# Kernel optimization log

Measured on AMD Instinct MI355X. Metric: run time of the kernel, lower is better.

The kernel has to match this reference:

```python
import jax, jax.numpy as jnp
import numpy as np

B, S = 256, 2048
VOCAB, E, H, OUT = 10, 32, 64, 10


def setup_inputs() -> dict:
    key = jax.random.key(0)
    ks = jax.random.split(key, 8)
    num1 = jax.random.randint(ks[0], (B, S), 0, VOCAB, dtype=jnp.int32)
    num2 = jax.random.randint(ks[1], (B, S), 0, VOCAB, dtype=jnp.int32)
    embed = jax.random.normal(ks[2], (VOCAB, E), dtype=jnp.float32) * 0.05
    Wx = jax.random.normal(ks[3], (2 * E, H), dtype=jnp.float32) * (1.0 / np.sqrt(2 * E))
    Wh = jax.random.normal(ks[4], (H, H), dtype=jnp.float32) * (1.0 / np.sqrt(H))
    b = jnp.zeros((H,), dtype=jnp.float32)
    Wd = jax.random.normal(ks[5], (H, OUT), dtype=jnp.float32) * (1.0 / np.sqrt(H))
    bd = jnp.zeros((OUT,), dtype=jnp.float32)
    return {"num1": num1, "num2": num2, "embed": embed, "Wx": Wx,
            "Wh": Wh, "b": b, "Wd": Wd, "bd": bd}


def reference(num1, num2, embed, Wx, Wh, b, Wd, bd):
    # embedding lookup + concat -> [B, S, 2E]
    x = jnp.concatenate([embed[num1], embed[num2]], axis=2)
    # precompute input projection once (big GEMM), scan only the recurrence
    xw = jnp.einsum('bse,eh->bsh', x, Wx) + b  # [B, S, H]

    def step(h, xw_t):
        h = jnp.tanh(xw_t + h @ Wh)  # SimpleRNNCell: tanh(x W + h U + b)
        return h, h

    h0 = jnp.zeros((x.shape[0], Wh.shape[0]), dtype=x.dtype)
    _, hs = jax.lax.scan(step, h0, jnp.swapaxes(xw, 0, 1))  # hs: [S, B, H]
    hs = jnp.swapaxes(hs, 0, 1)  # [B, S, H]
    logits = jnp.einsum('bsh,ho->bso', hs, Wd) + bd  # [B, S, 10]
    return logits
```

## Files before the change

### kernel.cpp

```cpp
#include <hip/hip_runtime.h>

namespace {
typedef float v2f __attribute__((ext_vector_type(2)));
typedef unsigned u32x2 __attribute__((ext_vector_type(2)));
constexpr int kB = 256;
constexpr int kS = 2048;
constexpr int kV = 10;
constexpr int kE = 32;
constexpr int kH = 64;
constexpr int kO = 10;
constexpr int kT = 16;
constexpr int kPad = 68;
constexpr int kTiles = kS / kT;
constexpr float kC = 2.885390081777927f;

__device__ __forceinline__ float step_tanh(float s) {
    s = __builtin_amdgcn_fmed3f(s, -26.f, 26.f);
    float e = __builtin_amdgcn_exp2f(s);
    float r = __builtin_amdgcn_rcpf(e + 1.f);
    return fmaf(-2.f, r, 1.f);
}

__device__ __forceinline__ float swap32(float p) {
    u32x2 r = __builtin_amdgcn_permlane32_swap(__float_as_uint(p),
                                               __float_as_uint(p),
                                               false, false);
    return (__uint_as_float(r.x) + __uint_as_float(r.y)) - p;
}

__device__ __forceinline__ void do_logits(const float* __restrict__ hb,
                                          const float (* __restrict__ WdT)[kPad],
                                          const float* __restrict__ bdL,
                                          float* __restrict__ out, int obase, int l)
{
    #pragma unroll
    for (int r = 0; r < 3; ++r) {
        int f = r * 64 + l;
        if (f < kT * kO) {
            int tl = f / kO;
            int o  = f - tl * kO;
            const float4* hb4 = reinterpret_cast<const float4*>(hb + tl * kPad);
            const float4* wd4 = reinterpret_cast<const float4*>(&WdT[o][0]);
            float a0 = bdL[o], a1 = 0.f, a2 = 0.f, a3 = 0.f;
            #pragma unroll
            for (int c = 0; c < kH / 4; ++c) {
                float4 h4 = hb4[c];
                float4 w4 = wd4[c];
                a0 = fmaf(h4.x, w4.x, a0);
                a1 = fmaf(h4.y, w4.y, a1);
                a2 = fmaf(h4.z, w4.z, a2);
                a3 = fmaf(h4.w, w4.w, a3);
            }
            out[obase + f] = (a0 + a1) + (a2 + a3);
        }
    }
}

__global__ __launch_bounds__(128, 1)
void rnn_fused(const int* __restrict__ num1, const int* __restrict__ num2,
               const float* __restrict__ embed, const float* __restrict__ Wx,
               const float* __restrict__ Wh, const float* __restrict__ bias,
               const float* __restrict__ Wd, const float* __restrict__ bd,
               float* __restrict__ out)
{
    const int row = blockIdx.x;
    const int tid = threadIdx.x;
    const int w   = tid >> 6;
    const int l   = tid & 63;
    const int lx  = l ^ 32;
    const int kbase = (l >> 5) * 32;

    __shared__ __align__(16) float TT[kV * kV][kH];
    __shared__ __align__(16) float hbuf[2][kT][kPad];
    __shared__ __align__(16) float WdT[kO][kPad];
    __shared__ float bdL[kO];

    v2f whcA2[kH / 4], whcB2[kH / 4];
    int idx_next = 0;
    const int lane16 = l & 15;
    const int nb = row * kS;
    const int orow = row * (kS * kO);

    if (w == 0) {
        float wxc[2 * kE];
        #pragma unroll
        for (int k = 0; k < 2 * kE; ++k) wxc[k] = Wx[k * kH + l];
        float bj = bias[l];
        float t1[kV], t2[kV];
        #pragma unroll
        for (int v = 0; v < kV; ++v) {
            float a0 = 0.f, a1 = 0.f;
            #pragma unroll
            for (int k = 0; k < kE; ++k) {
                float e = embed[v * kE + k];
                a0 = fmaf(e, wxc[k], a0);
                a1 = fmaf(e, wxc[kE + k], a1);
            }
            t1[v] = a0; t2[v] = a1;
        }
        #pragma unroll
        for (int v1 = 0; v1 < kV; ++v1)
            #pragma unroll
            for (int v2 = 0; v2 < kV; ++v2)
                TT[v1 * kV + v2][l] = kC * (t1[v1] + t2[v2] + bj);
        #pragma unroll
        for (int i = 0; i < kH / 4; ++i) {
            v2f ta, tb;
            ta.x = kC * Wh[(kbase + 2 * i)     * kH + l];
            ta.y = kC * Wh[(kbase + 2 * i + 1) * kH + l];
            tb.x = kC * Wh[(kbase + 2 * i)     * kH + lx];
            tb.y = kC * Wh[(kbase + 2 * i + 1) * kH + lx];
            whcA2[i] = ta; whcB2[i] = tb;
        }
        hbuf[1][kT - 1][l] = 0.f;
        idx_next = num1[nb + lane16] * kV + num2[nb + lane16];
        __builtin_amdgcn_s_setprio(1);
    } else {
        #pragma unroll
        for (int o = 0; o < kO; ++o) WdT[o][l] = Wd[l * kO + o];
        if (l < kO) bdL[l] = bd[l];
    }
    __syncthreads();

    const float* prevRow = &hbuf[1][kT - 1][0];

    for (int ti = 0; ti < kTiles; ++ti) {
        if (w == 0) {
            const int idxv = idx_next;
            if (ti + 1 < kTiles) {
                int tt = nb + (ti + 1) * kT + lane16;
                idx_next = num1[tt] * kV + num2[tt];
            }
            float* curBase = &hbuf[ti & 1][0][0];
            #pragma unroll 1
            for (int tl = 0; tl < kT; ++tl) {
                const int sidx = __builtin_amdgcn_readlane(idxv, tl);
                const float xwv = TT[sidx][l];
                const float4* hq = reinterpret_cast<const float4*>(prevRow + kbase);
                float4 q[8];
                #pragma unroll
                for (int c = 0; c < 8; ++c) q[c] = hq[c];
                __builtin_amdgcn_sched_barrier(0);
                v2f o0; o0.x = xwv; o0.y = 0.f;
                v2f o1 = {0.f, 0.f}, r0 = {0.f, 0.f}, r1 = {0.f, 0.f};
                #pragma unroll
                for (int c = 0; c < 8; ++c) {
                    v2f lo; lo.x = q[c].x; lo.y = q[c].y;
                    v2f hi; hi.x = q[c].z; hi.y = q[c].w;
                    o0 = lo * whcA2[2 * c]     + o0;
                    o1 = hi * whcA2[2 * c + 1] + o1;
                    r0 = lo * whcB2[2 * c]     + r0;
                    r1 = hi * whcB2[2 * c + 1] + r1;
                }
                v2f rv = r0 + r1;  float pPar = rv.x + rv.y;
                float oth = swap32(pPar);
                v2f ov = o0 + o1;  float pOwn = ov.x + ov.y;
                float hcur = step_tanh(pOwn + oth);
                float* wr = curBase + tl * kPad;
                wr[l] = hcur;
                prevRow = wr;
            }
        } else if (ti > 0) {
            do_logits(&hbuf[(ti - 1) & 1][0][0], WdT, bdL, out,
                      orow + (ti - 1) * kT * kO, l);
        }
        __syncthreads();
    }
    if (w == 1)
        do_logits(&hbuf[(kTiles - 1) & 1][0][0], WdT, bdL, out,
                  orow + (kS - kT) * kO, l);
}
}

extern "C" void kernel_launch(void* const* d_in, const int* in_sizes, int n_in,
                              void* d_out, int out_size, void* d_ws, size_t ws_size,
                              hipStream_t stream) {
    (void)in_sizes; (void)n_in; (void)d_ws; (void)ws_size; (void)out_size;
    rnn_fused<<<dim3(kB), dim3(128), 0, stream>>>(
        (const int*)d_in[0], (const int*)d_in[1],
        (const float*)d_in[2], (const float*)d_in[3],
        (const float*)d_in[4], (const float*)d_in[5],
        (const float*)d_in[6], (const float*)d_in[7],
        (float*)d_out);
}
```

Baseline: 456.2 us.

## Keep RNN hidden state in registers and exchange via DPP row rotations

Replaces the per-step write and re-read of the hidden state through shared memory with cross-lane exchanges. Each step rotates h within 16-lane rows using DPP row_ror. Partial sums are then combined with permlane16/permlane32 swaps. Wh is loaded into registers in a rotated layout to match the DPP pattern. The goal is to take LDS store-to-load latency off the serial recurrence critical path, at the cost of more cross-lane ops, more FMAs and select logic per step.

After: 509.7 us. 11.7% more time.

```diff
diff --git a/kernel.cpp b/kernel.cpp
--- a/kernel.cpp
+++ b/kernel.cpp
@@ -27,6 +27,21 @@
                                                false, false);
     return (__uint_as_float(r.x) + __uint_as_float(r.y)) - p;
 }
+
+#if __has_builtin(__builtin_amdgcn_permlane16_swap)
+__device__ __forceinline__ float sum16(float p) {
+    u32x2 r = __builtin_amdgcn_permlane16_swap(__float_as_uint(p),
+                                               __float_as_uint(p),
+                                               false, false);
+    return __uint_as_float(r.x) + __uint_as_float(r.y);
+}
+#else
+__device__ __forceinline__ float sum16(float p) {
+    float o = __int_as_float(
+        __builtin_amdgcn_ds_swizzle(__float_as_int(p), 0x401F));
+    return p + o;
+}
+#endif
 
 __device__ __forceinline__ void do_logits(const float* __restrict__ hb,
                                           const float (* __restrict__ WdT)[kPad],
@@ -67,17 +82,19 @@
     const int tid = threadIdx.x;
     const int w   = tid >> 6;
     const int l   = tid & 63;
-    const int lx  = l ^ 32;
-    const int kbase = (l >> 5) * 32;
+    const int b   = l & 15;
+    const int q   = l >> 4;
 
     __shared__ __align__(16) float TT[kV * kV][kH];
     __shared__ __align__(16) float hbuf[2][kT][kPad];
     __shared__ __align__(16) float WdT[kO][kPad];
     __shared__ float bdL[kO];
 
-    v2f whcA2[kH / 4], whcB2[kH / 4];
+    v2f wA[16], wB[16];
+    float h = 0.f;
     int idx_next = 0;
-    const int lane16 = l & 15;
+    bool qb0 = false, qb1 = false;
+    const int lane16 = b;
     const int nb = row * kS;
     const int orow = row * (kS * kO);
 
@@ -103,16 +120,22 @@
             #pragma unroll
             for (int v2 = 0; v2 < kV; ++v2)
                 TT[v1 * kV + v2][l] = kC * (t1[v1] + t2[v2] + bj);
-        #pragma unroll
-        for (int i = 0; i < kH / 4; ++i) {
-            v2f ta, tb;
-            ta.x = kC * Wh[(kbase + 2 * i)     * kH + l];
-            ta.y = kC * Wh[(kbase + 2 * i + 1) * kH + l];
-            tb.x = kC * Wh[(kbase + 2 * i)     * kH + lx];
-            tb.y = kC * Wh[(kbase + 2 * i + 1) * kH + lx];
-            whcA2[i] = ta; whcB2[i] = tb;
-        }
-        hbuf[1][kT - 1][l] = 0.f;
+
+        #define SETW(i, SRC)                                                \
+            do { int s_ = (SRC);                                            \
+                 const float* p_ = Wh + s_ * kH + b;                        \
+                 wA[i].x = kC * p_[0];  wA[i].y = kC * p_[16];              \
+                 wB[i].x = kC * p_[32]; wB[i].y = kC * p_[48]; } while (0)
+        SETW(0, l);
+        #define SETR(i) SETW(i, __builtin_amdgcn_mov_dpp(l, 0x120 + i, 0xf, 0xf, false))
+        SETR(1);  SETR(2);  SETR(3);  SETR(4);  SETR(5);
+        SETR(6);  SETR(7);  SETR(8);  SETR(9);  SETR(10);
+        SETR(11); SETR(12); SETR(13); SETR(14); SETR(15);
+        #undef SETR
+        #undef SETW
+
+        qb0 = (q & 1) != 0;
+        qb1 = (q & 2) != 0;
         idx_next = num1[nb + lane16] * kV + num2[nb + lane16];
         __builtin_amdgcn_s_setprio(1);
     } else {
@@ -121,8 +144,6 @@
         if (l < kO) bdL[l] = bd[l];
     }
     __syncthreads();
-
-    const float* prevRow = &hbuf[1][kT - 1][0];
 
     for (int ti = 0; ti < kTiles; ++ti) {
         if (w == 0) {
@@ -136,29 +157,35 @@
             for (int tl = 0; tl < kT; ++tl) {
                 const int sidx = __builtin_amdgcn_readlane(idxv, tl);
                 const float xwv = TT[sidx][l];
-                const float4* hq = reinterpret_cast<const float4*>(prevRow + kbase);
-                float4 q[8];
-                #pragma unroll
-                for (int c = 0; c < 8; ++c) q[c] = hq[c];
-                __builtin_amdgcn_sched_barrier(0);
-                v2f o0; o0.x = xwv; o0.y = 0.f;
-                v2f o1 = {0.f, 0.f}, r0 = {0.f, 0.f}, r1 = {0.f, 0.f};
-                #pragma unroll
-                for (int c = 0; c < 8; ++c) {
-                    v2f lo; lo.x = q[c].x; lo.y = q[c].y;
-                    v2f hi; hi.x = q[c].z; hi.y = q[c].w;
-                    o0 = lo * whcA2[2 * c]     + o0;
-                    o1 = hi * whcA2[2 * c + 1] + o1;
-                    r0 = lo * whcB2[2 * c]     + r0;
-                    r1 = hi * whcB2[2 * c + 1] + r1;
-                }
-                v2f rv = r0 + r1;  float pPar = rv.x + rv.y;
-                float oth = swap32(pPar);
-                v2f ov = o0 + o1;  float pOwn = ov.x + ov.y;
-                float hcur = step_tanh(pOwn + oth);
-                float* wr = curBase + tl * kPad;
-                wr[l] = hcur;
-                prevRow = wr;
+                v2f aA0, aA1, aB0, aB1;
+                { v2f h2; h2.x = h; h2.y = h;
+                  aA0 = h2 * wA[0]; aB0 = h2 * wB[0];
+                  aA1 = (v2f){0.f, 0.f}; aB1 = (v2f){0.f, 0.f}; }
+                #define MACI(i, AA, BB)                                     \
+                    do { float hr_ = __int_as_float(__builtin_amdgcn_mov_dpp( \
+                             __float_as_int(h), 0x120 + i, 0xf, 0xf, false)); \
+                         v2f h2_; h2_.x = hr_; h2_.y = hr_;                 \
+                         AA = h2_ * wA[i] + AA;                             \
+                         BB = h2_ * wB[i] + BB; } while (0)
+                MACI(1,  aA1, aB1); MACI(2,  aA0, aB0); MACI(3,  aA1, aB1);
+                MACI(4,  aA0, aB0); MACI(5,  aA1, aB1); MACI(6,  aA0, aB0);
+                MACI(7,  aA1, aB1); MACI(8,  aA0, aB0); MACI(9,  aA1, aB1);
+                MACI(10, aA0, aB0); MACI(11, aA1, aB1); MACI(12, aA0, aB0);
+                MACI(13, aA1, aB1); MACI(14, aA0, aB0); MACI(15, aA1, aB1);
+                #undef MACI
+                v2f a01 = aA0 + aA1;
+                v2f a23 = aB0 + aB1;
+                float T0 = sum16(a01.x);
+                float T1 = sum16(a01.y);
+                float T2 = sum16(a23.x);
+                float T3 = sum16(a23.y);
+                float sA = qb0 ? T1 : T0;
+                float sB = qb0 ? T3 : T2;
+                float Tq  = qb1 ? sB : sA;
+                float Tq2 = qb1 ? sA : sB;
+                float oth = swap32(Tq2);
+                h = step_tanh((Tq + oth) + xwv);
+                curBase[tl * kPad + l] = h;
             }
         } else if (ti > 0) {
             do_logits(&hbuf[(ti - 1) & 1][0][0], WdT, bdL, out,
```
